# Optimization experiments

Measured on AMD Instinct MI355X. Metric: run time of the kernel, lower is better.

Reference implementation:

```python
import jax, jax.numpy as jnp
import numpy as np

N_NODES = 10000
SEQ_LEN = 50


def setup_inputs() -> dict:
    key = jax.random.key(0)
    ks = jax.random.split(key, 12)
    B, IN, H, E = 2, 128, 64, 160000
    s = 0.05
    return {
        "x": jax.random.normal(ks[0], (B, IN), jnp.float32),
        "src": jax.random.randint(ks[1], (E,), 0, N_NODES, jnp.int32),
        "dst": jax.random.randint(ks[2], (E,), 0, N_NODES, jnp.int32),
        "w_r_w": jax.random.normal(ks[3], (IN, H), jnp.float32) * s,
        "w_r_b": jnp.zeros((H,), jnp.float32),
        "w_z_w": jax.random.normal(ks[4], (IN, H), jnp.float32) * s,
        "w_z_b": jnp.zeros((H,), jnp.float32),
        "w_h_w": jax.random.normal(ks[5], (IN, H), jnp.float32) * s,
        "w_h_b": jnp.zeros((H,), jnp.float32),
        "gcn_w": jax.random.normal(ks[6], (H, H), jnp.float32) * s,
        "gcn_b": jnp.zeros((H,), jnp.float32),
    }


def reference(x, src, dst, w_r_w, w_r_b, w_z_w, w_z_b, w_h_w, w_h_b, gcn_w, gcn_b):
    B = x.shape[0]
    H = gcn_w.shape[0]
    N = N_NODES
    ones = jnp.ones(src.shape, jnp.float32)
    deg_out = jax.ops.segment_sum(ones, src, num_segments=N)
    deg_in = jax.ops.segment_sum(ones, dst, num_segments=N)
    norm_s = jnp.clip(deg_out, 1.0) ** -0.5  # [N]
    norm_d = jnp.clip(deg_in, 1.0) ** -0.5   # [N]

    def gcn(h):  # h: [B, N, H] -> symmetric-normalized GraphConv (DGL norm='both')
        hs = h * norm_s[None, :, None]
        msg = jnp.take(hs, src, axis=1).swapaxes(0, 1)        # [E, B, H]
        agg = jax.ops.segment_sum(msg, dst, num_segments=N)   # [N, B, H]
        agg = (agg * norm_d[:, None, None]).swapaxes(0, 1)    # [B, N, H]
        return agg @ gcn_w + gcn_b

    # time-invariant input projections (x is fixed across timesteps)
    xr = (x @ w_r_w + w_r_b)[:, None, :]  # [B, 1, H]
    xz = (x @ w_z_w + w_z_b)[:, None, :]
    xh = (x @ w_h_w + w_h_b)[:, None, :]

    h0 = jnp.zeros((B, N, H), jnp.float32)

    def step(h, _):
        g = gcn(h)  # identical for all three gate uses
        r = jax.nn.sigmoid(xr + g)
        z = jax.nn.sigmoid(xz + g)
        h_tilde = jnp.tanh(xh + r * g)
        h_new = (1.0 - z) * h + z * h_tilde
        return h_new, h_new

    _, outs = jax.lax.scan(step, h0, None, length=SEQ_LEN)  # [T, B, N, H]
    return outs.transpose(1, 0, 2, 3)                        # [B, T, N, H]
```

## Files before the change

### kernel.cpp

```cpp
#include <hip/hip_runtime.h>
#include <cstdint>
#include <cstddef>

#define NNODES 10000
#define HDIM 64
#define BDIM 2
#define INDIM 128
#define TSTEPS 50

__device__ __forceinline__ float sigmoidf_(float x){ return 1.0f/(1.0f+__expf(-x)); }
__device__ __forceinline__ float tanhf_(float x){ float e=__expf(2.0f*x); return 1.0f-2.0f/(e+1.0f); }

__device__ __forceinline__ uint32_t pack_bf16x2(float a, float b){
  uint32_t ua = __float_as_uint(a), ub = __float_as_uint(b);
  ua = (ua + 0x7fffu + ((ua>>16)&1u)) >> 16;
  ub = (ub + 0x7fffu + ((ub>>16)&1u)) >> 16;
  return ua | (ub<<16);
}

__global__ void hist_kernel(const int* __restrict__ src, const int* __restrict__ dst,
                            int* __restrict__ deg_out, int* __restrict__ deg_in, int E){
  int e = blockIdx.x*blockDim.x + threadIdx.x;
  if (e < E){
    atomicAdd(&deg_out[src[e]], 1);
    atomicAdd(&deg_in[dst[e]], 1);
  }
}

__global__ void scan_kernel(const int* __restrict__ deg_in, const int* __restrict__ deg_out,
                            int* __restrict__ row_off, int* __restrict__ cursor,
                            float* __restrict__ norm_s, float* __restrict__ norm_d){
  __shared__ int part[256];
  int tid = threadIdx.x;
  const int CH = (NNODES + 255)/256;
  int base = tid*CH;
  int local = 0;
  for (int k=0;k<CH;k++){ int n=base+k; if(n<NNODES) local += (deg_in[n]+7)&~7; }
  part[tid]=local;
  __syncthreads();
  if (tid==0){
    int run=0;
    for(int i=0;i<256;i++){ int t=part[i]; part[i]=run; run+=t; }
  }
  __syncthreads();
  int run = part[tid];
  for (int k=0;k<CH;k++){
    int n=base+k;
    if (n<NNODES){
      int di = deg_in[n];
      row_off[n]=run; cursor[n]=run;
      run += (di+7)&~7;
      norm_d[n] = rsqrtf(fmaxf((float)di,1.0f));
      norm_s[n] = rsqrtf(fmaxf((float)deg_out[n],1.0f));
    }
  }
  if (tid==255) row_off[NNODES]=run;
}

__global__ void fill_kernel(const int* __restrict__ src, const int* __restrict__ dst,
                            int* __restrict__ cursor, int* __restrict__ csr, int E){
  int e = blockIdx.x*blockDim.x + threadIdx.x;
  if (e<E){
    int pos = atomicAdd(&cursor[dst[e]],1);
    csr[pos] = src[e];
  }
}

__global__ void pad_kernel(const int* __restrict__ row_off, const int* __restrict__ cursor,
                           int* __restrict__ csr){
  int n = blockIdx.x*blockDim.x + threadIdx.x;
  if (n < NNODES){
    int q  = cursor[n];
    int qe = row_off[n+1];
    for (; q < qe; ++q) csr[q] = NNODES;
  }
}

__global__ void xproj_kernel(const float* __restrict__ x,
                             const float* __restrict__ wr, const float* __restrict__ br,
                             const float* __restrict__ wz, const float* __restrict__ bz,
                             const float* __restrict__ wh, const float* __restrict__ bh,
                             float* __restrict__ xproj){
  int tid = threadIdx.x;
  if (tid >= 384) return;
  int g = tid >> 7; int r = tid & 127; int b = r >> 6; int i = r & 63;
  const float* w  = (g==0)?wr:(g==1)?wz:wh;
  const float* bb = (g==0)?br:(g==1)?bz:bh;
  float s = bb[i];
  for (int k=0;k<INDIM;k++) s = fmaf(x[b*INDIM+k], w[k*HDIM+i], s);
  xproj[g*128 + i*2 + b] = s;
}

__global__ void transpose_w_kernel(const float* __restrict__ gcn_w, float* __restrict__ wT){
  int tid = threadIdx.x;
  for (int k=0;k<16;k++){
    int idx = tid*16 + k;
    int i = idx >> 6, j = idx & 63;
    wT[idx] = gcn_w[j*HDIM + i];
  }
}

__launch_bounds__(512, 6)
__global__ void step_kernel(const float2* __restrict__ h_in, float2* __restrict__ h_out,
                            const uint32_t* __restrict__ yb_in, uint32_t* __restrict__ yb_out,
                            float* __restrict__ out, int t,
                            const int* __restrict__ row_off, const int* __restrict__ csr,
                            const float* __restrict__ norm_d, const float* __restrict__ norm_s,
                            const float* __restrict__ wT, const float* __restrict__ gcn_b,
                            const float2* __restrict__ xproj){
  __shared__ __align__(16) float4 wlds[64][16];
  __shared__ __align__(16) float2 hstage[8][64];

  const int tid  = threadIdx.x;
  const int lane = tid & 63;
  const int wv   = tid >> 6;

  {
    const float4* wt4 = (const float4*)wT;
    #pragma unroll
    for (int q=0;q<2;q++){
      int c = tid*2 + q;
      int l = c >> 4, k = c & 15;
      int sl = (l & 15) ^ (((l>>4)&1) << 2);
      wlds[l][k ^ sl] = wt4[c];
    }
  }

  const int n   = __builtin_amdgcn_readfirstlane(blockIdx.x*8 + wv);
  const int beg = __builtin_amdgcn_readfirstlane(row_off[n]);
  const int end = __builtin_amdgcn_readfirstlane(row_off[n+1]);

  __syncthreads();

  float2 hold = h_in[(size_t)n*HDIM + lane];

  const uint32_t lane_u = (uint32_t)lane;
  float2 a0{0.f,0.f}, a1{0.f,0.f}, a2{0.f,0.f}, a3{0.f,0.f};
  const int4* cp = (const int4*)(csr + beg);
  int nIt = (end - beg) >> 3;
  #pragma unroll 1
  for (int it=0; it<nIt; ++it){
    int4 ca = cp[2*it];
    int4 cb = cp[2*it+1];
    uint32_t p0 = yb_in[(uint32_t)ca.x*HDIM + lane_u];
    uint32_t p1 = yb_in[(uint32_t)ca.y*HDIM + lane_u];
    uint32_t p2 = yb_in[(uint32_t)ca.z*HDIM + lane_u];
    uint32_t p3 = yb_in[(uint32_t)ca.w*HDIM + lane_u];
    uint32_t p4 = yb_in[(uint32_t)cb.x*HDIM + lane_u];
    uint32_t p5 = yb_in[(uint32_t)cb.y*HDIM + lane_u];
    uint32_t p6 = yb_in[(uint32_t)cb.z*HDIM + lane_u];
    uint32_t p7 = yb_in[(uint32_t)cb.w*HDIM + lane_u];
    a0.x += __uint_as_float(p0<<16); a0.y += __uint_as_float(p0 & 0xffff0000u);
    a1.x += __uint_as_float(p1<<16); a1.y += __uint_as_float(p1 & 0xffff0000u);
    a2.x += __uint_as_float(p2<<16); a2.y += __uint_as_float(p2 & 0xffff0000u);
    a3.x += __uint_as_float(p3<<16); a3.y += __uint_as_float(p3 & 0xffff0000u);
    a0.x += __uint_as_float(p4<<16); a0.y += __uint_as_float(p4 & 0xffff0000u);
    a1.x += __uint_as_float(p5<<16); a1.y += __uint_as_float(p5 & 0xffff0000u);
    a2.x += __uint_as_float(p6<<16); a2.y += __uint_as_float(p6 & 0xffff0000u);
    a3.x += __uint_as_float(p7<<16); a3.y += __uint_as_float(p7 & 0xffff0000u);
  }
  float s0 = (a0.x + a1.x) + (a2.x + a3.x);
  float s1 = (a0.y + a1.y) + (a2.y + a3.y);

  const float nd   = norm_d[n];
  const float ns   = norm_s[n];
  const float bias = gcn_b[lane];
  const float2 xrv = xproj[lane];
  const float2 xzv = xproj[64+lane];
  const float2 xhv = xproj[128+lane];

  float g0 = fmaf(nd, s0, bias);
  float g1 = fmaf(nd, s1, bias);

  float r0 = sigmoidf_(xrv.x + g0), r1 = sigmoidf_(xrv.y + g1);
  float z0 = sigmoidf_(xzv.x + g0), z1 = sigmoidf_(xzv.y + g1);
  float t0 = tanhf_(xhv.x + r0*g0), t1 = tanhf_(xhv.y + r1*g1);
  float hn0 = hold.x + z0*(t0 - hold.x);
  float hn1 = hold.y + z1*(t1 - hold.y);

  const size_t NH = (size_t)NNODES*HDIM;
  h_out[(size_t)n*HDIM + lane] = make_float2(hn0,hn1);
  size_t idx = (size_t)t*NH + (size_t)n*HDIM + lane;
  __builtin_nontemporal_store(hn0, &out[idx]);
  __builtin_nontemporal_store(hn1, &out[(size_t)TSTEPS*NH + idx]);

  hstage[wv][lane] = make_float2(hn0,hn1);
  __asm__ volatile("s_waitcnt lgkmcnt(0)" ::: "memory");

  const int sl = (lane & 15) ^ (((lane>>4)&1) << 2);
  const float4* hp = (const float4*)hstage[wv];
  float y0 = 0.f, y1 = 0.f;
  #pragma unroll
  for (int k=0;k<16;k++){
    float4 w4 = wlds[lane][k ^ sl];
    float4 ha = hp[2*k];
    float4 hb = hp[2*k+1];
    y0 = fmaf(w4.x, ha.x, y0); y1 = fmaf(w4.x, ha.y, y1);
    y0 = fmaf(w4.y, ha.z, y0); y1 = fmaf(w4.y, ha.w, y1);
    y0 = fmaf(w4.z, hb.x, y0); y1 = fmaf(w4.z, hb.y, y1);
    y0 = fmaf(w4.w, hb.z, y0); y1 = fmaf(w4.w, hb.w, y1);
  }
  yb_out[(size_t)n*HDIM + lane] = pack_bf16x2(ns*y0, ns*y1);
}

extern "C" void kernel_launch(void* const* d_in, const int* in_sizes, int n_in,
                              void* d_out, int out_size, void* d_ws, size_t ws_size,
                              hipStream_t stream){
  const float* x   = (const float*)d_in[0];
  const int*   src = (const int*)d_in[1];
  const int*   dst = (const int*)d_in[2];
  const float* wr  = (const float*)d_in[3];
  const float* br  = (const float*)d_in[4];
  const float* wz  = (const float*)d_in[5];
  const float* bz  = (const float*)d_in[6];
  const float* wh  = (const float*)d_in[7];
  const float* bh  = (const float*)d_in[8];
  const float* gw  = (const float*)d_in[9];
  const float* gb  = (const float*)d_in[10];
  float* out = (float*)d_out;
  const int E = in_sizes[1];

  char* ws = (char*)d_ws;
  size_t o = 0;
  int*   deg_out = (int*)(ws+o);  o += 10240*4;
  int*   deg_in  = (int*)(ws+o);  o += 10240*4;
  int*   cursor  = (int*)(ws+o);  o += 10240*4;
  int*   row_off = (int*)(ws+o);  o += 10256*4;
  float* norm_s  = (float*)(ws+o); o += 10240*4;
  float* norm_d  = (float*)(ws+o); o += 10240*4;
  const size_t CSRCAP = (size_t)E + 7*NNODES + 16;
  int*   csr     = (int*)(ws+o);  o += ((CSRCAP*4 + 15) & ~(size_t)15);
  float* xproj   = (float*)(ws+o); o += 512*4;
  float* wT      = (float*)(ws+o); o += 4096*4;
  o = (o + 255) & ~(size_t)255;
  const size_t NHf2 = (size_t)NNODES*HDIM*sizeof(float2);
  const size_t NYB  = (size_t)(NNODES+1)*HDIM*sizeof(uint32_t);
  float2*   h0  = (float2*)(ws+o);   o += NHf2;
  uint32_t* yb0 = (uint32_t*)(ws+o); o += NYB;
  uint32_t* yb1 = (uint32_t*)(ws+o); o += NYB;
  float2*   h1  = (float2*)(ws+o);   o += NHf2;

  hipMemsetAsync(deg_out, 0, 2*10240*4, stream);
  hipMemsetAsync(h0, 0, NHf2 + 2*NYB, stream);

  int eb = (E+255)/256;
  hist_kernel<<<eb,256,0,stream>>>(src,dst,deg_out,deg_in,E);
  scan_kernel<<<1,256,0,stream>>>(deg_in,deg_out,row_off,cursor,norm_s,norm_d);
  fill_kernel<<<eb,256,0,stream>>>(src,dst,cursor,csr,E);
  pad_kernel<<<(NNODES+255)/256,256,0,stream>>>(row_off,cursor,csr);
  xproj_kernel<<<1,384,0,stream>>>(x,wr,br,wz,bz,wh,bh,xproj);
  transpose_w_kernel<<<1,256,0,stream>>>(gw,wT);

  float2* hin = h0;  float2* hout = h1;
  uint32_t* ybin = yb0; uint32_t* ybout = yb1;
  for (int t=0;t<TSTEPS;t++){
    step_kernel<<<1250,512,0,stream>>>(hin,hout,ybin,ybout,out,t,row_off,csr,
                                       norm_d,norm_s,wT,gb,(const float2*)xproj);
    float2* tf = hin; hin = hout; hout = tf;
    uint32_t* tb = ybin; ybin = ybout; ybout = tb;
  }
}
```

Baseline: 991.2 us.

## Process two nodes per wavefront and store CSR as precomputed byte offsets

Each wavefront now handles two nodes (n and n+5000), interleaving their neighbor gathers so more independent loads are in flight, and the grid is halved to match. The CSR entries are stored as byte offsets (src*256), which removes the index multiply from the gather address computation. The per-wave LDS staging and the matvec now cover two nodes, sharing each weight read across both. The cost is higher register pressure and fewer blocks for the GPU to spread across CUs, with imbalance where the two rows differ in length.

```diff
diff --git a/kernel.cpp b/kernel.cpp
--- a/kernel.cpp
+++ b/kernel.cpp
@@ -4,7 +4,6 @@
 
 #define NNODES 10000
 #define HDIM 64
-#define BDIM 2
 #define INDIM 128
 #define TSTEPS 50
 
@@ -58,21 +57,21 @@
 }
 
 __global__ void fill_kernel(const int* __restrict__ src, const int* __restrict__ dst,
-                            int* __restrict__ cursor, int* __restrict__ csr, int E){
+                            int* __restrict__ cursor, uint32_t* __restrict__ csrb, int E){
   int e = blockIdx.x*blockDim.x + threadIdx.x;
   if (e<E){
     int pos = atomicAdd(&cursor[dst[e]],1);
-    csr[pos] = src[e];
+    csrb[pos] = (uint32_t)src[e]*256u;
   }
 }
 
 __global__ void pad_kernel(const int* __restrict__ row_off, const int* __restrict__ cursor,
-                           int* __restrict__ csr){
+                           uint32_t* __restrict__ csrb){
   int n = blockIdx.x*blockDim.x + threadIdx.x;
   if (n < NNODES){
     int q  = cursor[n];
     int qe = row_off[n+1];
-    for (; q < qe; ++q) csr[q] = NNODES;
+    for (; q < qe; ++q) csrb[q] = (uint32_t)NNODES*256u;
   }
 }
 
@@ -100,16 +99,38 @@
   }
 }
 
+#define ACC8(A0,A1,A2,A3,q0,q1,q2,q3,q4,q5,q6,q7) do{ \
+  A0.x += __uint_as_float((q0)<<16); A0.y += __uint_as_float((q0)&0xffff0000u); \
+  A1.x += __uint_as_float((q1)<<16); A1.y += __uint_as_float((q1)&0xffff0000u); \
+  A2.x += __uint_as_float((q2)<<16); A2.y += __uint_as_float((q2)&0xffff0000u); \
+  A3.x += __uint_as_float((q3)<<16); A3.y += __uint_as_float((q3)&0xffff0000u); \
+  A0.x += __uint_as_float((q4)<<16); A0.y += __uint_as_float((q4)&0xffff0000u); \
+  A1.x += __uint_as_float((q5)<<16); A1.y += __uint_as_float((q5)&0xffff0000u); \
+  A2.x += __uint_as_float((q6)<<16); A2.y += __uint_as_float((q6)&0xffff0000u); \
+  A3.x += __uint_as_float((q7)<<16); A3.y += __uint_as_float((q7)&0xffff0000u); \
+}while(0)
+
+#define GATHER8(cp,it,P0,P1,P2,P3,P4,P5,P6,P7) \
+  uint4 oa##P0 = (cp)[2*(it)], ob##P0 = (cp)[2*(it)+1]; \
+  uint32_t P0 = *(const uint32_t*)(ybb+oa##P0.x); \
+  uint32_t P1 = *(const uint32_t*)(ybb+oa##P0.y); \
+  uint32_t P2 = *(const uint32_t*)(ybb+oa##P0.z); \
+  uint32_t P3 = *(const uint32_t*)(ybb+oa##P0.w); \
+  uint32_t P4 = *(const uint32_t*)(ybb+ob##P0.x); \
+  uint32_t P5 = *(const uint32_t*)(ybb+ob##P0.y); \
+  uint32_t P6 = *(const uint32_t*)(ybb+ob##P0.z); \
+  uint32_t P7 = *(const uint32_t*)(ybb+ob##P0.w);
+
 __launch_bounds__(512, 6)
 __global__ void step_kernel(const float2* __restrict__ h_in, float2* __restrict__ h_out,
                             const uint32_t* __restrict__ yb_in, uint32_t* __restrict__ yb_out,
                             float* __restrict__ out, int t,
-                            const int* __restrict__ row_off, const int* __restrict__ csr,
+                            const int* __restrict__ row_off, const uint32_t* __restrict__ csrb,
                             const float* __restrict__ norm_d, const float* __restrict__ norm_s,
                             const float* __restrict__ wT, const float* __restrict__ gcn_b,
                             const float2* __restrict__ xproj){
   __shared__ __align__(16) float4 wlds[64][16];
-  __shared__ __align__(16) float2 hstage[8][64];
+  __shared__ __align__(16) float2 hstage[8][2][64];
 
   const int tid  = threadIdx.x;
   const int lane = tid & 63;
@@ -120,87 +141,110 @@
     #pragma unroll
     for (int q=0;q<2;q++){
       int c = tid*2 + q;
-      int l = c >> 4, k = c & 15;
-      int sl = (l & 15) ^ (((l>>4)&1) << 2);
-      wlds[l][k ^ sl] = wt4[c];
+      int l = c >> 4, kk = c & 15;
+      int swl = (l & 15) ^ (((l>>4)&1) << 2);
+      wlds[l][kk ^ swl] = wt4[c];
     }
   }
 
-  const int n   = __builtin_amdgcn_readfirstlane(blockIdx.x*8 + wv);
-  const int beg = __builtin_amdgcn_readfirstlane(row_off[n]);
-  const int end = __builtin_amdgcn_readfirstlane(row_off[n+1]);
-
+  const int wid = __builtin_amdgcn_readfirstlane(blockIdx.x*8 + wv);
+  const int n0 = wid, n1 = wid + 5000;
+
+  int beg0 = __builtin_amdgcn_readfirstlane(row_off[n0]);
+  int end0 = __builtin_amdgcn_readfirstlane(row_off[n0+1]);
+  int beg1 = __builtin_amdgcn_readfirstlane(row_off[n1]);
+  int end1 = __builtin_amdgcn_readfirstlane(row_off[n1+1]);
+
+  float2 hold0 = h_in[(size_t)n0*HDIM + lane];
+  float2 hold1 = h_in[(size_t)n1*HDIM + lane];
+
+  const char* ybb = (const char*)yb_in + (uint32_t)(lane*4);
+  const uint4* cp0 = (const uint4*)(csrb + beg0);
+  const uint4* cp1 = (const uint4*)(csrb + beg1);
+  const int it0 = (end0-beg0)>>3;
+  const int it1 = (end1-beg1)>>3;
+  const int itc = it0 < it1 ? it0 : it1;
+
+  float2 A0{0.f,0.f},A1{0.f,0.f},A2{0.f,0.f},A3{0.f,0.f};
+  float2 B0{0.f,0.f},B1{0.f,0.f},B2{0.f,0.f},B3{0.f,0.f};
+
+  int it = 0;
+  #pragma unroll 1
+  for (; it<itc; ++it){
+    GATHER8(cp0,it,p0,p1,p2,p3,p4,p5,p6,p7);
+    GATHER8(cp1,it,q0,q1,q2,q3,q4,q5,q6,q7);
+    ACC8(A0,A1,A2,A3,p0,p1,p2,p3,p4,p5,p6,p7);
+    ACC8(B0,B1,B2,B3,q0,q1,q2,q3,q4,q5,q6,q7);
+  }
+  #pragma unroll 1
+  for (int ia=it; ia<it0; ++ia){
+    GATHER8(cp0,ia,p0,p1,p2,p3,p4,p5,p6,p7);
+    ACC8(A0,A1,A2,A3,p0,p1,p2,p3,p4,p5,p6,p7);
+  }
+  #pragma unroll 1
+  for (int ib=it; ib<it1; ++ib){
+    GATHER8(cp1,ib,q0,q1,q2,q3,q4,q5,q6,q7);
+    ACC8(B0,B1,B2,B3,q0,q1,q2,q3,q4,q5,q6,q7);
+  }
+
+  float s00 = (A0.x+A1.x)+(A2.x+A3.x), s01 = (A0.y+A1.y)+(A2.y+A3.y);
+  float s10 = (B0.x+B1.x)+(B2.x+B3.x), s11 = (B0.y+B1.y)+(B2.y+B3.y);
+
+  const float  bias = gcn_b[lane];
+  const float2 xrv  = xproj[lane];
+  const float2 xzv  = xproj[64+lane];
+  const float2 xhv  = xproj[128+lane];
+  const float  nd0  = norm_d[n0], ns0 = norm_s[n0];
+  const float  nd1  = norm_d[n1], ns1 = norm_s[n1];
+
+  float g00 = fmaf(nd0, s00, bias), g01 = fmaf(nd0, s01, bias);
+  float g10 = fmaf(nd1, s10, bias), g11 = fmaf(nd1, s11, bias);
+
+  float r00 = sigmoidf_(xrv.x+g00), r01 = sigmoidf_(xrv.y+g01);
+  float r10 = sigmoidf_(xrv.x+g10), r11 = sigmoidf_(xrv.y+g11);
+  float z00 = sigmoidf_(xzv.x+g00), z01 = sigmoidf_(xzv.y+g01);
+  float z10 = sigmoidf_(xzv.x+g10), z11 = sigmoidf_(xzv.y+g11);
+  float t00 = tanhf_(xhv.x+r00*g00), t01 = tanhf_(xhv.y+r01*g01);
+  float t10 = tanhf_(xhv.x+r10*g10), t11 = tanhf_(xhv.y+r11*g11);
+  float h00 = hold0.x + z00*(t00 - hold0.x);
+  float h01 = hold0.y + z01*(t01 - hold0.y);
+  float h10 = hold1.x + z10*(t10 - hold1.x);
+  float h11 = hold1.y + z11*(t11 - hold1.y);
+
+  const size_t NH = (size_t)NNODES*HDIM;
+  h_out[(size_t)n0*HDIM + lane] = make_float2(h00,h01);
+  h_out[(size_t)n1*HDIM + lane] = make_float2(h10,h11);
+  size_t idx0 = (size_t)t*NH + (size_t)n0*HDIM + lane;
+  size_t idx1 = (size_t)t*NH + (size_t)n1*HDIM + lane;
+  __builtin_nontemporal_store(h00, &out[idx0]);
+  __builtin_nontemporal_store(h01, &out[(size_t)TSTEPS*NH + idx0]);
+  __builtin_nontemporal_store(h10, &out[idx1]);
+  __builtin_nontemporal_store(h11, &out[(size_t)TSTEPS*NH + idx1]);
+
+  hstage[wv][0][lane] = make_float2(h00,h01);
+  hstage[wv][1][lane] = make_float2(h10,h11);
   __syncthreads();
 
-  float2 hold = h_in[(size_t)n*HDIM + lane];
-
-  const uint32_t lane_u = (uint32_t)lane;
-  float2 a0{0.f,0.f}, a1{0.f,0.f}, a2{0.f,0.f}, a3{0.f,0.f};
-  const int4* cp = (const int4*)(csr + beg);
-  int nIt = (end - beg) >> 3;
-  #pragma unroll 1
-  for (int it=0; it<nIt; ++it){
-    int4 ca = cp[2*it];
-    int4 cb = cp[2*it+1];
-    uint32_t p0 = yb_in[(uint32_t)ca.x*HDIM + lane_u];
-    uint32_t p1 = yb_in[(uint32_t)ca.y*HDIM + lane_u];
-    uint32_t p2 = yb_in[(uint32_t)ca.z*HDIM + lane_u];
-    uint32_t p3 = yb_in[(uint32_t)ca.w*HDIM + lane_u];
-    uint32_t p4 = yb_in[(uint32_t)cb.x*HDIM + lane_u];
-    uint32_t p5 = yb_in[(uint32_t)cb.y*HDIM + lane_u];
-    uint32_t p6 = yb_in[(uint32_t)cb.z*HDIM + lane_u];
-    uint32_t p7 = yb_in[(uint32_t)cb.w*HDIM + lane_u];
-    a0.x += __uint_as_float(p0<<16); a0.y += __uint_as_float(p0 & 0xffff0000u);
-    a1.x += __uint_as_float(p1<<16); a1.y += __uint_as_float(p1 & 0xffff0000u);
-    a2.x += __uint_as_float(p2<<16); a2.y += __uint_as_float(p2 & 0xffff0000u);
-    a3.x += __uint_as_float(p3<<16); a3.y += __uint_as_float(p3 & 0xffff0000u);
-    a0.x += __uint_as_float(p4<<16); a0.y += __uint_as_float(p4 & 0xffff0000u);
-    a1.x += __uint_as_float(p5<<16); a1.y += __uint_as_float(p5 & 0xffff0000u);
-    a2.x += __uint_as_float(p6<<16); a2.y += __uint_as_float(p6 & 0xffff0000u);
-    a3.x += __uint_as_float(p7<<16); a3.y += __uint_as_float(p7 & 0xffff0000u);
-  }
-  float s0 = (a0.x + a1.x) + (a2.x + a3.x);
-  float s1 = (a0.y + a1.y) + (a2.y + a3.y);
-
-  const float nd   = norm_d[n];
-  const float ns   = norm_s[n];
-  const float bias = gcn_b[lane];
-  const float2 xrv = xproj[lane];
-  const float2 xzv = xproj[64+lane];
-  const float2 xhv = xproj[128+lane];
-
-  float g0 = fmaf(nd, s0, bias);
-  float g1 = fmaf(nd, s1, bias);
-
-  float r0 = sigmoidf_(xrv.x + g0), r1 = sigmoidf_(xrv.y + g1);
-  float z0 = sigmoidf_(xzv.x + g0), z1 = sigmoidf_(xzv.y + g1);
-  float t0 = tanhf_(xhv.x + r0*g0), t1 = tanhf_(xhv.y + r1*g1);
-  float hn0 = hold.x + z0*(t0 - hold.x);
-  float hn1 = hold.y + z1*(t1 - hold.y);
-
-  const size_t NH = (size_t)NNODES*HDIM;
-  h_out[(size_t)n*HDIM + lane] = make_float2(hn0,hn1);
-  size_t idx = (size_t)t*NH + (size_t)n*HDIM + lane;
-  __builtin_nontemporal_store(hn0, &out[idx]);
-  __builtin_nontemporal_store(hn1, &out[(size_t)TSTEPS*NH + idx]);
-
-  hstage[wv][lane] = make_float2(hn0,hn1);
-  __asm__ volatile("s_waitcnt lgkmcnt(0)" ::: "memory");
-
   const int sl = (lane & 15) ^ (((lane>>4)&1) << 2);
-  const float4* hp = (const float4*)hstage[wv];
-  float y0 = 0.f, y1 = 0.f;
+  const float4* hp0 = (const float4*)hstage[wv][0];
+  const float4* hp1 = (const float4*)hstage[wv][1];
+  float y00=0.f, y01=0.f, y10=0.f, y11=0.f;
   #pragma unroll
-  for (int k=0;k<16;k++){
-    float4 w4 = wlds[lane][k ^ sl];
-    float4 ha = hp[2*k];
-    float4 hb = hp[2*k+1];
-    y0 = fmaf(w4.x, ha.x, y0); y1 = fmaf(w4.x, ha.y, y1);
-    y0 = fmaf(w4.y, ha.z, y0); y1 = fmaf(w4.y, ha.w, y1);
-    y0 = fmaf(w4.z, hb.x, y0); y1 = fmaf(w4.z, hb.y, y1);
-    y0 = fmaf(w4.w, hb.z, y0); y1 = fmaf(w4.w, hb.w, y1);
-  }
-  yb_out[(size_t)n*HDIM + lane] = pack_bf16x2(ns*y0, ns*y1);
+  for (int kk=0;kk<16;kk++){
+    float4 w4  = wlds[lane][kk ^ sl];
+    float4 ha0 = hp0[2*kk], hb0 = hp0[2*kk+1];
+    float4 ha1 = hp1[2*kk], hb1 = hp1[2*kk+1];
+    y00 = fmaf(w4.x, ha0.x, y00); y01 = fmaf(w4.x, ha0.y, y01);
+    y10 = fmaf(w4.x, ha1.x, y10); y11 = fmaf(w4.x, ha1.y, y11);
+    y00 = fmaf(w4.y, ha0.z, y00); y01 = fmaf(w4.y, ha0.w, y01);
+    y10 = fmaf(w4.y, ha1.z, y10); y11 = fmaf(w4.y, ha1.w, y11);
+    y00 = fmaf(w4.z, hb0.x, y00); y01 = fmaf(w4.z, hb0.y, y01);
+    y10 = fmaf(w4.z, hb1.x, y10); y11 = fmaf(w4.z, hb1.y, y11);
+    y00 = fmaf(w4.w, hb0.z, y00); y01 = fmaf(w4.w, hb0.w, y01);
+    y10 = fmaf(w4.w, hb1.z, y10); y11 = fmaf(w4.w, hb1.w, y11);
+  }
+  yb_out[(uint32_t)n0*HDIM + lane] = pack_bf16x2(ns0*y00, ns0*y01);
+  yb_out[(uint32_t)n1*HDIM + lane] = pack_bf16x2(ns1*y10, ns1*y11);
 }
 
 extern "C" void kernel_launch(void* const* d_in, const int* in_sizes, int n_in,
@@ -229,33 +273,33 @@
   float* norm_s  = (float*)(ws+o); o += 10240*4;
   float* norm_d  = (float*)(ws+o); o += 10240*4;
   const size_t CSRCAP = (size_t)E + 7*NNODES + 16;
-  int*   csr     = (int*)(ws+o);  o += ((CSRCAP*4 + 15) & ~(size_t)15);
+  uint32_t* csrb = (uint32_t*)(ws+o);  o += ((CSRCAP*4 + 15) & ~(size_t)15);
   float* xproj   = (float*)(ws+o); o += 512*4;
   float* wT      = (float*)(ws+o); o += 4096*4;
   o = (o + 255) & ~(size_t)255;
   const size_t NHf2 = (size_t)NNODES*HDIM*sizeof(float2);
   const size_t NYB  = (size_t)(NNODES+1)*HDIM*sizeof(uint32_t);
-  float2*   h0  = (float2*)(ws+o);   o += NHf2;
   uint32_t* yb0 = (uint32_t*)(ws+o); o += NYB;
   uint32_t* yb1 = (uint32_t*)(ws+o); o += NYB;
+  float2*   h0  = (float2*)(ws+o);   o += NHf2;
   float2*   h1  = (float2*)(ws+o);   o += NHf2;
 
   hipMemsetAsync(deg_out, 0, 2*10240*4, stream);
-  hipMemsetAsync(h0, 0, NHf2 + 2*NYB, stream);
+  hipMemsetAsync(yb0, 0, 2*NYB + NHf2, stream);
 
   int eb = (E+255)/256;
   hist_kernel<<<eb,256,0,stream>>>(src,dst,deg_out,deg_in,E);
   scan_kernel<<<1,256,0,stream>>>(deg_in,deg_out,row_off,cursor,norm_s,norm_d);
-  fill_kernel<<<eb,256,0,stream>>>(src,dst,cursor,csr,E);
-  pad_kernel<<<(NNODES+255)/256,256,0,stream>>>(row_off,cursor,csr);
+  fill_kernel<<<eb,256,0,stream>>>(src,dst,cursor,csrb,E);
+  pad_kernel<<<(NNODES+255)/256,256,0,stream>>>(row_off,cursor,csrb);
   xproj_kernel<<<1,384,0,stream>>>(x,wr,br,wz,bz,wh,bh,xproj);
   transpose_w_kernel<<<1,256,0,stream>>>(gw,wT);
 
   float2* hin = h0;  float2* hout = h1;
   uint32_t* ybin = yb0; uint32_t* ybout = yb1;
   for (int t=0;t<TSTEPS;t++){
-    step_kernel<<<1250,512,0,stream>>>(hin,hout,ybin,ybout,out,t,row_off,csr,
-                                       norm_d,norm_s,wT,gb,(const float2*)xproj);
+    step_kernel<<<625,512,0,stream>>>(hin,hout,ybin,ybout,out,t,row_off,csrb,
+                                      norm_d,norm_s,wT,gb,(const float2*)xproj);
     float2* tf = hin; hin = hout; hout = tf;
     uint32_t* tb = ybin; ybin = ybout; ybout = tb;
   }
```

After: 989.5 us. About the same (-0.2%).
